# Performance work log

Hardware: AMD Instinct MI355X
Metric: run time of the kernel (lower is better)

Reference implementation:

```python
import jax, jax.numpy as jnp
import numpy as np
import math

N, D, H, O = 8192, 2048, 512, 32


def setup_inputs() -> dict:
    key = jax.random.key(0)
    k0, k1, k2, k3 = jax.random.split(key, 4)
    x = jax.random.normal(k0, (N, D), jnp.float32)
    y = jax.random.normal(k1, (N, O), jnp.float32)
    # kaiming_uniform fan_in / relu: bound = sqrt(6 / fan_in)
    b_w1 = math.sqrt(6.0 / D)
    W1 = jax.random.uniform(k2, (H, D), jnp.float32, -b_w1, b_w1)
    b1 = jnp.full((H,), 0.01, jnp.float32)
    # W = [final_layer.weight^T ; bias] -> (H+1, O)
    b_w2 = math.sqrt(6.0 / H)
    W = jax.random.uniform(k3, (H + 1, O), jnp.float32, -b_w2, b_w2)
    P = jnp.eye(H + 1, dtype=jnp.float32)  # P = 1 * I
    return {"x": x, "y": y, "W1": W1, "b1": b1, "W": W, "P": P, "epoch": 2}


def _rls(Phi, y, W, P):
    """Sequential Sherman-Morrison rank-1 updates (the torch per-sample loop) as lax.scan."""
    def step(carry, inp):
        W, P = carry
        xi, yi = inp                      # xi: (H+1,), yi: (O,)
        px = P @ xi                       # (H+1,)
        denom = 1.0 + xi @ px             # scalar 1 + xi P xi^T
        W = W - jnp.outer(px, xi @ W - yi) / denom
        P = P - jnp.outer(px, xi @ P) / denom
        return (W, P), None
    (W, P), _ = jax.lax.scan(step, (W, P), (Phi, y))
    return W, P


def reference(x, y, W1, b1, W, P, epoch):
    # feature_extractor: Linear + ReLU
    feature = jax.nn.relu(x @ W1.T + b1)                       # (N, H)
    ones_col = jnp.ones((feature.shape[0], 1), feature.dtype)
    Phi = jnp.concatenate([feature, ones_col], axis=1)         # (N, H+1)
    # RLS processes ceil(0.5**epoch * N) samples (deterministic prefix here)
    sample = math.ceil(0.5 ** epoch * Phi.shape[0])
    W_new, P_new = _rls(Phi[:sample], y[:sample], W, P)
    # final_layer with updated weights: out = feature @ W_new[:-1] + W_new[-1] == Phi @ W_new
    out = Phi @ W_new                                          # (N, O)
    return out
```

## Files before the change

kernel.cpp:

```cpp
#include <hip/hip_runtime.h>
#include <math.h>

#define NROWS 8192
#define DIN   2048
#define HF    512
#define NAUG  513
#define OOUT  32
#define SRLS  2048
#define LDP   576
#define NPAD  576

typedef short bf16x8 __attribute__((ext_vector_type(8)));
typedef float f32x4  __attribute__((ext_vector_type(4)));

__global__ __launch_bounds__(256) void split32(const float* __restrict__ s,
                                               unsigned short* __restrict__ hi,
                                               unsigned short* __restrict__ lo,
                                               int n4)
{
    int stride = gridDim.x * blockDim.x;
    for (int i = blockIdx.x * blockDim.x + threadIdx.x; i < n4; i += stride) {
        float4 v = ((const float4*)s)[i];
        float vv[4] = {v.x, v.y, v.z, v.w};
        ushort4 h, l;
        unsigned short hh[4], ll[4];
#pragma unroll
        for (int j = 0; j < 4; ++j) {
            unsigned int bits = __float_as_uint(vv[j]);
            float hf = __uint_as_float(bits & 0xFFFF0000u);
            float rf = vv[j] - hf;
            hh[j] = (unsigned short)(bits >> 16);
            ll[j] = (unsigned short)(__float_as_uint(rf) >> 16);
        }
        h.x = hh[0]; h.y = hh[1]; h.z = hh[2]; h.w = hh[3];
        l.x = ll[0]; l.y = ll[1]; l.z = ll[2]; l.w = ll[3];
        ((ushort4*)hi)[i] = h;
        ((ushort4*)lo)[i] = l;
    }
}

__device__ __forceinline__ void gl_lds16(const unsigned short* g, unsigned short* l)
{
    __builtin_amdgcn_global_load_lds(
        (const __attribute__((address_space(1))) unsigned int*)g,
        (__attribute__((address_space(3))) unsigned int*)l, 16, 0, 0);
}

__global__ __launch_bounds__(256) void phi_mfma(const unsigned short* __restrict__ Ahi,
                                                const unsigned short* __restrict__ Alo,
                                                const unsigned short* __restrict__ Bhi,
                                                const unsigned short* __restrict__ Blo,
                                                const float* __restrict__ b1,
                                                float* __restrict__ Phi)
{
    __shared__ unsigned short sAhi[128 * 32], sAlo[128 * 32];
    __shared__ unsigned short sBhi[64 * 32],  sBlo[64 * 32];
    const int tid = threadIdx.x;
    const int bx = blockIdx.x & 7;
    const int by = blockIdx.x >> 3;
    const int row0 = by * 128, col0 = bx * 64;
    const int wave = tid >> 6, lane = tid & 63;
    const int wr = wave >> 1, wc = wave & 1;
    const int sr = tid >> 2, sk = (tid & 3) * 8;

    f32x4 acc[4][2] = {};

    for (int k0 = 0; k0 < DIN; k0 += 32) {
        gl_lds16(&Ahi[(size_t)(row0 + sr) * DIN + k0 + sk],      &sAhi[sr * 32 + sk]);
        gl_lds16(&Ahi[(size_t)(row0 + 64 + sr) * DIN + k0 + sk], &sAhi[(64 + sr) * 32 + sk]);
        gl_lds16(&Alo[(size_t)(row0 + sr) * DIN + k0 + sk],      &sAlo[sr * 32 + sk]);
        gl_lds16(&Alo[(size_t)(row0 + 64 + sr) * DIN + k0 + sk], &sAlo[(64 + sr) * 32 + sk]);
        gl_lds16(&Bhi[(size_t)(col0 + sr) * DIN + k0 + sk],      &sBhi[sr * 32 + sk]);
        gl_lds16(&Blo[(size_t)(col0 + sr) * DIN + k0 + sk],      &sBlo[sr * 32 + sk]);
        __syncthreads();

        const int rA = lane & 15;
        const int ko = (lane >> 4) * 8;
        bf16x8 ah[4], al[4], bh[2], bl[2];
#pragma unroll
        for (int m = 0; m < 4; ++m) {
            int r = wr * 64 + m * 16 + rA;
            ah[m] = *(const bf16x8*)&sAhi[r * 32 + ko];
            al[m] = *(const bf16x8*)&sAlo[r * 32 + ko];
        }
#pragma unroll
        for (int n = 0; n < 2; ++n) {
            int cC = wc * 32 + n * 16 + rA;
            bh[n] = *(const bf16x8*)&sBhi[cC * 32 + ko];
            bl[n] = *(const bf16x8*)&sBlo[cC * 32 + ko];
        }
#pragma unroll
        for (int m = 0; m < 4; ++m)
#pragma unroll
            for (int n = 0; n < 2; ++n) {
                acc[m][n] = __builtin_amdgcn_mfma_f32_16x16x32_bf16(ah[m], bh[n], acc[m][n], 0, 0, 0);
                acc[m][n] = __builtin_amdgcn_mfma_f32_16x16x32_bf16(ah[m], bl[n], acc[m][n], 0, 0, 0);
                acc[m][n] = __builtin_amdgcn_mfma_f32_16x16x32_bf16(al[m], bh[n], acc[m][n], 0, 0, 0);
            }
        __syncthreads();
    }

#pragma unroll
    for (int n = 0; n < 2; ++n) {
        int col = col0 + wc * 32 + n * 16 + (lane & 15);
        float bb = b1[col];
#pragma unroll
        for (int m = 0; m < 4; ++m) {
            int rbase = row0 + wr * 64 + m * 16 + (lane >> 4) * 4;
#pragma unroll
            for (int r = 0; r < 4; ++r) {
                float v = acc[m][n][r] + bb;
                Phi[(size_t)(rbase + r) * LDP + col] = fmaxf(v, 0.0f);
            }
        }
    }
}

__global__ void aux_fill(const float* __restrict__ y, float* __restrict__ Phi)
{
    int idx = blockIdx.x * blockDim.x + threadIdx.x;
    int r = idx >> 6;
    int c = 512 + (idx & 63);
    float v = 0.0f;
    if (c == 512) v = 1.0f;
    else if (c >= 513 && c < 513 + OOUT && r < SRLS) v = y[r * OOUT + (c - 513)];
    Phi[(size_t)r * LDP + c] = v;
}

__global__ __launch_bounds__(256) void gram(const float* __restrict__ Phi,
                                            float* __restrict__ G)
{
    int bi = blockIdx.x / 18, bj = blockIdx.x % 18;
    if (bi > bj) return;
    __shared__ float Ta[32][33];
    __shared__ float Tb[32][33];
    const int tid = threadIdx.x;
    const int tx = tid & 15, ty = tid >> 4;
    const int i0 = bi * 32, j0 = bj * 32;
    double acc00 = 0., acc01 = 0., acc10 = 0., acc11 = 0.;

    for (int s0 = 0; s0 < SRLS; s0 += 32) {
        int r = tid >> 3, c4 = (tid & 7) * 4;
        float4 va = *(const float4*)&Phi[(size_t)(s0 + r) * LDP + i0 + c4];
        Ta[r][c4 + 0] = va.x; Ta[r][c4 + 1] = va.y;
        Ta[r][c4 + 2] = va.z; Ta[r][c4 + 3] = va.w;
        float4 vb = *(const float4*)&Phi[(size_t)(s0 + r) * LDP + j0 + c4];
        Tb[r][c4 + 0] = vb.x; Tb[r][c4 + 1] = vb.y;
        Tb[r][c4 + 2] = vb.z; Tb[r][c4 + 3] = vb.w;
        __syncthreads();
#pragma unroll
        for (int s = 0; s < 32; ++s) {
            double a0 = (double)Ta[s][ty * 2], a1 = (double)Ta[s][ty * 2 + 1];
            double b0 = (double)Tb[s][tx * 2], b1v = (double)Tb[s][tx * 2 + 1];
            acc00 += a0 * b0; acc01 += a0 * b1v;
            acc10 += a1 * b0; acc11 += a1 * b1v;
        }
        __syncthreads();
    }
    double accs[2][2] = {{acc00, acc01}, {acc10, acc11}};
#pragma unroll
    for (int ii = 0; ii < 2; ++ii)
#pragma unroll
        for (int jj = 0; jj < 2; ++jj) {
            int gi = i0 + ty * 2 + ii, gj = j0 + tx * 2 + jj;
            float v = (float)(accs[ii][jj] + ((gi == gj) ? 1.0 : 0.0));
            G[gi * NPAD + gj] = v;
            G[gj * NPAD + gi] = v;
        }
}

__global__ void gd_fill(const float* __restrict__ G, double* __restrict__ Gd)
{
    int idx = blockIdx.x * blockDim.x + threadIdx.x;
    int i = idx / NPAD, j = idx - i * NPAD;
    double v;
    if (i < NAUG && j < NAUG) v = (double)G[idx];
    else v = (i == j) ? 1.0 : 0.0;
    Gd[idx] = v;
}

__global__ void bd_fill(const float* __restrict__ G, const float* __restrict__ W0,
                        double* __restrict__ Bd)
{
    int idx = blockIdx.x * blockDim.x + threadIdx.x;
    int i = idx >> 5, c = idx & 31;
    double v = 0.0;
    if (i < NAUG) v = (double)G[i * NPAD + 513 + c] + (double)W0[i * OOUT + c];
    Bd[idx] = v;
}

__global__ __launch_bounds__(256) void chol_diag(double* __restrict__ Gd,
                                                 double* __restrict__ Dinv, int p)
{
    __shared__ double A[64][65];
    __shared__ double Zs[64][65];
    const int tid = threadIdx.x;
    const int r0g = p * 64;
    for (int idx = tid; idx < 4096; idx += 256) {
        int r = idx >> 6, c = idx & 63;
        A[r][c] = Gd[(size_t)(r0g + r) * NPAD + r0g + c];
    }
    __syncthreads();

    for (int kb = 0; kb < 8; ++kb) {
        const int k0 = kb * 8;
        if (tid < 64) {
            const int lane = tid;
            for (int k = k0; k < k0 + 8; ++k) {
                double d = A[k][k];
                double inv = 1.0 / sqrt(d);
                double lik = 0.0;
                if (lane == k)     A[k][k] = d * inv;
                else if (lane > k) { lik = A[lane][k] * inv; A[lane][k] = lik; }
                asm volatile("" ::: "memory");
                if (lane > k) {
                    for (int j = k + 1; j < k0 + 8; ++j)
                        A[lane][j] -= lik * A[j][k];
                }
                asm volatile("" ::: "memory");
            }
        }
        __syncthreads();
        if (k0 + 8 < 64) {
            const int i = tid >> 2, cg = tid & 3;
            if (i >= k0 + 8) {
                double lik[8];
#pragma unroll
                for (int k = 0; k < 8; ++k) lik[k] = A[i][k0 + k];
                for (int j = k0 + 8 + cg; j <= i; j += 4) {
                    double s = A[i][j];
#pragma unroll
                    for (int k = 0; k < 8; ++k) s -= lik[k] * A[j][k0 + k];
                    A[i][j] = s;
                }
            }
        }
        __syncthreads();
    }

    for (int rb = 0; rb < 8; ++rb) {
        const int r0 = rb * 8;
        const int c = tid & 63, pg = tid >> 6;
        double t0 = 0.0, t1 = 0.0;
        for (int q = 0; q < r0; ++q) {
            double zqc = Zs[q][c];
            t0 += A[r0 + pg][q] * zqc;
            t1 += A[r0 + pg + 4][q] * zqc;
        }
        Zs[r0 + pg][c]     = ((r0 + pg) == c ? 1.0 : 0.0) - t0;
        Zs[r0 + pg + 4][c] = ((r0 + pg + 4) == c ? 1.0 : 0.0) - t1;
        __syncthreads();
        if (tid < 64) {
            const int lane = tid;
            for (int q = 0; q < 8; ++q) {
                double v = Zs[r0 + q][lane];
                for (int w = 0; w < q; ++w) v -= A[r0 + q][r0 + w] * Zs[r0 + w][lane];
                Zs[r0 + q][lane] = v / A[r0 + q][r0 + q];
                asm volatile("" ::: "memory");
            }
        }
        __syncthreads();
    }

    for (int idx = tid; idx < 4096; idx += 256) {
        int r = idx >> 6, c = idx & 63;
        Gd[(size_t)(r0g + r) * NPAD + r0g + c] = A[r][c];
        Dinv[(size_t)p * 4096 + idx] = (c <= r) ? Zs[r][c] : 0.0;
    }
}

__global__ __launch_bounds__(256) void trsm(double* __restrict__ Gd,
                                            const double* __restrict__ Dinv, int p)
{
    __shared__ double As[64][65];
    __shared__ double Mi[64][65];
    const int tid = threadIdx.x;
    const int rb = p + 1 + blockIdx.x;
    const int d0 = p * 64, r0 = rb * 64;
    const double* Dv = Dinv + (size_t)p * 4096;
    for (int idx = tid; idx < 4096; idx += 256) {
        int r = idx >> 6, c = idx & 63;
        As[r][c] = Gd[(size_t)(r0 + r) * NPAD + d0 + c];
        Mi[r][c] = Dv[idx];
    }
    __syncthreads();
    const int tx = tid & 15, ty = tid >> 4;
    double acc[4][4] = {};
    for (int q = 0; q < 64; ++q) {
        double av[4], mv[4];
#pragma unroll
        for (int u = 0; u < 4; ++u) av[u] = As[ty * 4 + u][q];
#pragma unroll
        for (int v = 0; v < 4; ++v) mv[v] = Mi[tx * 4 + v][q];
#pragma unroll
        for (int u = 0; u < 4; ++u)
#pragma unroll
            for (int v = 0; v < 4; ++v) acc[u][v] += av[u] * mv[v];
    }
    __syncthreads();
#pragma unroll
    for (int u = 0; u < 4; ++u)
#pragma unroll
        for (int v = 0; v < 4; ++v)
            Gd[(size_t)(r0 + ty * 4 + u) * NPAD + d0 + tx * 4 + v] = acc[u][v];
}

__global__ __launch_bounds__(256) void syrk(double* __restrict__ Gd, int p)
{
    __shared__ double LiT[64][66];
    __shared__ double LjT[64][66];
    const int m = 8 - p;
    int b = blockIdx.x, jj = 0;
    while (b >= m - jj) { b -= m - jj; ++jj; }
    const int jb = p + 1 + jj, ib = jb + b;
    const int i0 = ib * 64, j0 = jb * 64, d0 = p * 64;
    const int tid = threadIdx.x;
    for (int idx = tid; idx < 4096; idx += 256) {
        int r = idx >> 6, c = idx & 63;
        LiT[c][r] = Gd[(size_t)(i0 + r) * NPAD + d0 + c];
        LjT[c][r] = Gd[(size_t)(j0 + r) * NPAD + d0 + c];
    }
    __syncthreads();
    const int tx = tid & 15, ty = tid >> 4;
    const int rr = ty * 4, cc = tx * 4;
    double acc[4][4] = {};
    for (int k = 0; k < 64; ++k) {
        double ai[4], aj[4];
#pragma unroll
        for (int q = 0; q < 4; ++q) ai[q] = LiT[k][rr + q];
#pragma unroll
        for (int q = 0; q < 4; ++q) aj[q] = LjT[k][cc + q];
#pragma unroll
        for (int q = 0; q < 4; ++q)
#pragma unroll
            for (int w = 0; w < 4; ++w) acc[q][w] += ai[q] * aj[w];
    }
#pragma unroll
    for (int q = 0; q < 4; ++q)
#pragma unroll
        for (int w = 0; w < 4; ++w) {
            size_t off = (size_t)(i0 + rr + q) * NPAD + j0 + cc + w;
            Gd[off] -= acc[q][w];
        }
}

__global__ __launch_bounds__(256) void mnprep(const double* __restrict__ Gd,
                                              const double* __restrict__ Dinv,
                                              double* __restrict__ Mb,
                                              double* __restrict__ Nb)
{
    __shared__ double Ls[64][65];
    __shared__ double Ds[64][65];
    int b = blockIdx.x;
    const bool doN = (b >= 36);
    if (doN) b -= 36;
    int jj = 0, rem = b;
    while (rem >= 8 - jj) { rem -= 8 - jj; ++jj; }
    const int ii = jj + 1 + rem;
    const int tid = threadIdx.x;
    const double* Dv = Dinv + (size_t)(doN ? ii : jj) * 4096;
    for (int idx = tid; idx < 4096; idx += 256) {
        int r = idx >> 6, c = idx & 63;
        Ls[r][c] = Gd[(size_t)(ii * 64 + r) * NPAD + jj * 64 + c];
        Ds[r][c] = Dv[idx];
    }
    __syncthreads();
    const int tx = tid & 15, ty = tid >> 4;
    double acc[4][4] = {};
    for (int k = 0; k < 64; ++k) {
        double a[4], bb[4];
        if (!doN) {
#pragma unroll
            for (int u = 0; u < 4; ++u) a[u]  = Ls[ty * 4 + u][k];
#pragma unroll
            for (int v = 0; v < 4; ++v) bb[v] = Ds[k][tx * 4 + v];
        } else {
#pragma unroll
            for (int u = 0; u < 4; ++u) a[u]  = Ds[ty * 4 + u][k];
#pragma unroll
            for (int v = 0; v < 4; ++v) bb[v] = Ls[k][tx * 4 + v];
        }
#pragma unroll
        for (int u = 0; u < 4; ++u)
#pragma unroll
            for (int v = 0; v < 4; ++v) acc[u][v] += a[u] * bb[v];
    }
    double* dst = (doN ? Nb : Mb) + (size_t)(ii * 9 + jj) * 4096;
#pragma unroll
    for (int u = 0; u < 4; ++u)
#pragma unroll
        for (int v = 0; v < 4; ++v)
            dst[(ty * 4 + u) * 64 + tx * 4 + v] = acc[u][v];
}

__global__ __launch_bounds__(256) void fwd_step(const double* __restrict__ Mb,
                                                double* __restrict__ Bd, int j)
{
    __shared__ double Ms[64][65];
    __shared__ double Bj[64][33];
    const int i = j + 1 + blockIdx.x;
    const int tid = threadIdx.x;
    const double* Mblk = Mb + (size_t)(i * 9 + j) * 4096;
    for (int idx = tid; idx < 4096; idx += 256) Ms[idx >> 6][idx & 63] = Mblk[idx];
    for (int idx = tid; idx < 2048; idx += 256) Bj[idx >> 5][idx & 31] = Bd[j * 2048 + idx];
    __syncthreads();
    const int c = tid & 31, rg = tid >> 5;
    double acc[8] = {};
    for (int k = 0; k < 64; ++k) {
        double bk = Bj[k][c];
#pragma unroll
        for (int u = 0; u < 8; ++u) acc[u] += Ms[rg * 8 + u][k] * bk;
    }
#pragma unroll
    for (int u = 0; u < 8; ++u)
        Bd[(size_t)(i * 64 + rg * 8 + u) * 32 + c] -= acc[u];
}

__global__ __launch_bounds__(256) void ydiag(const double* __restrict__ Dinv,
                                             double* __restrict__ Bd)
{
    __shared__ double Ds[64][65];
    __shared__ double Bi[64][33];
    const int i = blockIdx.x;
    const int tid = threadIdx.x;
    const double* Dv = Dinv + (size_t)i * 4096;
    for (int idx = tid; idx < 4096; idx += 256) Ds[idx >> 6][idx & 63] = Dv[idx];
    for (int idx = tid; idx < 2048; idx += 256) Bi[idx >> 5][idx & 31] = Bd[i * 2048 + idx];
    __syncthreads();
    const int c = tid & 31, rg = tid >> 5;
    double acc[8] = {};
    for (int k = 0; k < 64; ++k) {
        double bk = Bi[k][c];
#pragma unroll
        for (int u = 0; u < 8; ++u) acc[u] += Ds[rg * 8 + u][k] * bk;
    }
#pragma unroll
    for (int u = 0; u < 8; ++u)
        Bd[(size_t)(i * 64 + rg * 8 + u) * 32 + c] = acc[u];
}

__global__ __launch_bounds__(256) void bwd_step(const double* __restrict__ Nb,
                                                double* __restrict__ Bd, int q)
{
    __shared__ double Ns[64][65];
    __shared__ double Bq[64][33];
    const int i = blockIdx.x;
    const int tid = threadIdx.x;
    const double* Nblk = Nb + (size_t)(q * 9 + i) * 4096;
    for (int idx = tid; idx < 4096; idx += 256) Ns[idx >> 6][idx & 63] = Nblk[idx];
    for (int idx = tid; idx < 2048; idx += 256) Bq[idx >> 5][idx & 31] = Bd[q * 2048 + idx];
    __syncthreads();
    const int c = tid & 31, rg = tid >> 5;
    double acc[8] = {};
    for (int k = 0; k < 64; ++k) {
        double bk = Bq[k][c];
#pragma unroll
        for (int u = 0; u < 8; ++u) acc[u] += Ns[k][rg * 8 + u] * bk;
    }
#pragma unroll
    for (int u = 0; u < 8; ++u)
        Bd[(size_t)(i * 64 + rg * 8 + u) * 32 + c] -= acc[u];
}

__global__ __launch_bounds__(256) void xfinal(const double* __restrict__ Dinv,
                                              const double* __restrict__ Bd,
                                              float* __restrict__ Xs)
{
    __shared__ double Ds[64][65];
    __shared__ double Bi[64][33];
    const int i = blockIdx.x;
    const int tid = threadIdx.x;
    const double* Dv = Dinv + (size_t)i * 4096;
    for (int idx = tid; idx < 4096; idx += 256) Ds[idx >> 6][idx & 63] = Dv[idx];
    for (int idx = tid; idx < 2048; idx += 256) Bi[idx >> 5][idx & 31] = Bd[i * 2048 + idx];
    __syncthreads();
    const int c = tid & 31, rg = tid >> 5;
    double acc[8] = {};
    for (int k = 0; k < 64; ++k) {
        double bk = Bi[k][c];
#pragma unroll
        for (int u = 0; u < 8; ++u) acc[u] += Ds[k][rg * 8 + u] * bk;
    }
#pragma unroll
    for (int u = 0; u < 8; ++u) {
        int gi = i * 64 + rg * 8 + u;
        if (gi < NAUG) Xs[gi * 32 + c] = (float)acc[u];
    }
}

__global__ __launch_bounds__(256) void out_gemm(const float* __restrict__ Phi,
                                                const float* __restrict__ Xs,
                                                float* __restrict__ outp)
{
    __shared__ float sX[NAUG * 32];
    const int tid = threadIdx.x;
    for (int i2 = tid; i2 < NAUG * 32; i2 += 256) sX[i2] = Xs[i2];
    __syncthreads();
    int rt = tid >> 5, c = tid & 31;
    int i0 = blockIdx.x * 32;
    for (int i = i0 + rt; i < i0 + 32; i += 8) {
        const float* prow = &Phi[(size_t)i * LDP];
        float acc = 0.0f;
        for (int k = 0; k < 512; k += 4) {
            float4 p = *(const float4*)&prow[k];
            acc = fmaf(p.x, sX[(k + 0) * 32 + c], acc);
            acc = fmaf(p.y, sX[(k + 1) * 32 + c], acc);
            acc = fmaf(p.z, sX[(k + 2) * 32 + c], acc);
            acc = fmaf(p.w, sX[(k + 3) * 32 + c], acc);
        }
        acc = fmaf(prow[512], sX[512 * 32 + c], acc);
        outp[(size_t)i * 32 + c] = acc;
    }
}

extern "C" void kernel_launch(void* const* d_in, const int* in_sizes, int n_in,
                              void* d_out, int out_size, void* d_ws, size_t ws_size,
                              hipStream_t stream)
{
    const float* x  = (const float*)d_in[0];
    const float* y  = (const float*)d_in[1];
    const float* W1 = (const float*)d_in[2];
    const float* b1 = (const float*)d_in[3];
    const float* W0 = (const float*)d_in[4];

    char* base = (char*)d_ws;
    float*  Phi  = (float*)base;
    float*  G    = (float*)(base + 18874368);
    double* Gd   = (double*)(base + 20201472);
    double* Bd   = (double*)(base + 22855680);
    double* Dinv = (double*)(base + 23003136);
    float*  Xs   = (float*)(base + 23298048);
    double* Mb   = (double*)(base + 23367680);
    double* Nb   = (double*)(base + 26021888);
    unsigned short* xhi = (unsigned short*)(base + 28676096);
    unsigned short* xlo = (unsigned short*)(base + 62230528);
    unsigned short* whi = (unsigned short*)(base + 95784960);
    unsigned short* wlo = (unsigned short*)(base + 97882112);
    float* outp = (float*)d_out;

    split32<<<2048, 256, 0, stream>>>(x,  xhi, xlo, NROWS * DIN / 4);
    split32<<<1024, 256, 0, stream>>>(W1, whi, wlo, HF * DIN / 4);
    phi_mfma<<<512, 256, 0, stream>>>(xhi, xlo, whi, wlo, b1, Phi);
    aux_fill<<<(NROWS * 64) / 256, 256, 0, stream>>>(y, Phi);
    gram<<<18 * 18, 256, 0, stream>>>(Phi, G);
    gd_fill<<<(NPAD * NPAD) / 256, 256, 0, stream>>>(G, Gd);
    bd_fill<<<(NPAD * 32) / 256, 256, 0, stream>>>(G, W0, Bd);
    for (int p = 0; p < 9; ++p) {
        chol_diag<<<1, 256, 0, stream>>>(Gd, Dinv, p);
        int m = 8 - p;
        if (m > 0) {
            trsm<<<m, 256, 0, stream>>>(Gd, Dinv, p);
            syrk<<<m * (m + 1) / 2, 256, 0, stream>>>(Gd, p);
        }
    }
    mnprep<<<72, 256, 0, stream>>>(Gd, Dinv, Mb, Nb);
    for (int j = 0; j < 8; ++j)
        fwd_step<<<8 - j, 256, 0, stream>>>(Mb, Bd, j);
    ydiag<<<9, 256, 0, stream>>>(Dinv, Bd);
    for (int q = 8; q >= 1; --q)
        bwd_step<<<q, 256, 0, stream>>>(Nb, Bd, q);
    xfinal<<<9, 256, 0, stream>>>(Dinv, Bd, Xs);
    out_gemm<<<NROWS / 32, 256, 0, stream>>>(Phi, Xs, outp);
}
```

Baseline: 1.121 ms.

## Split gram across sample chunks, fuse trsm+syrk, single-kernel triangular sweeps

The Gram matrix is now computed as 8 sample-chunk partials over lower-triangle tiles plus a y-projection tile, then reduced in a separate kernel straight into the double-precision buffer. This replaces the serial single-pass gram and its conversion kernels. The per-panel trsm and syrk launches are fused into one panel_up kernel that keeps the L blocks in a separate buffer. The diagonal Cholesky factor uses shuffles and register arrays. The forward and backward block sweeps, previously about 18 small launches, become one 1024-thread kernel, trading launch overhead for single-CU serial execution.

```diff
diff --git a/kernel.cpp b/kernel.cpp
--- a/kernel.cpp
+++ b/kernel.cpp
@@ -116,35 +116,47 @@
     }
 }
 
-__global__ void aux_fill(const float* __restrict__ y, float* __restrict__ Phi)
+__global__ void aux_fill(float* __restrict__ Phi)
+{
+    int r = blockIdx.x * blockDim.x + threadIdx.x;
+    if (r < NROWS) Phi[(size_t)r * LDP + 512] = 1.0f;
+}
+
+__global__ void gd_init(double* __restrict__ Gd)
 {
     int idx = blockIdx.x * blockDim.x + threadIdx.x;
-    int r = idx >> 6;
-    int c = 512 + (idx & 63);
-    float v = 0.0f;
-    if (c == 512) v = 1.0f;
-    else if (c >= 513 && c < 513 + OOUT && r < SRLS) v = y[r * OOUT + (c - 513)];
-    Phi[(size_t)r * LDP + c] = v;
-}
-
-__global__ __launch_bounds__(256) void gram(const float* __restrict__ Phi,
-                                            float* __restrict__ G)
-{
-    int bi = blockIdx.x / 18, bj = blockIdx.x % 18;
-    if (bi > bj) return;
+    int i = idx / NPAD, j = idx - i * NPAD;
+    Gd[idx] = (i == j) ? 1.0 : 0.0;
+}
+
+__global__ __launch_bounds__(256) void gram_part(const float* __restrict__ Phi,
+                                                 const float* __restrict__ y,
+                                                 double* __restrict__ Gp)
+{
+    const int pr = blockIdx.x % 170;
+    const int ch = blockIdx.x / 170;
     __shared__ float Ta[32][33];
     __shared__ float Tb[32][33];
     const int tid = threadIdx.x;
     const int tx = tid & 15, ty = tid >> 4;
-    const int i0 = bi * 32, j0 = bj * 32;
+    int i0, j0; bool ytile;
+    if (pr < 153) {
+        int rem = pr, bj = 0;
+        while (rem >= 17 - bj) { rem -= 17 - bj; ++bj; }
+        int bi = bj + rem;
+        i0 = bi * 32; j0 = bj * 32; ytile = false;
+    } else {
+        i0 = (pr - 153) * 32; j0 = 0; ytile = true;
+    }
     double acc00 = 0., acc01 = 0., acc10 = 0., acc11 = 0.;
-
-    for (int s0 = 0; s0 < SRLS; s0 += 32) {
+    const int sBase = ch * 256;
+    for (int s0 = sBase; s0 < sBase + 256; s0 += 32) {
         int r = tid >> 3, c4 = (tid & 7) * 4;
         float4 va = *(const float4*)&Phi[(size_t)(s0 + r) * LDP + i0 + c4];
         Ta[r][c4 + 0] = va.x; Ta[r][c4 + 1] = va.y;
         Ta[r][c4 + 2] = va.z; Ta[r][c4 + 3] = va.w;
-        float4 vb = *(const float4*)&Phi[(size_t)(s0 + r) * LDP + j0 + c4];
+        float4 vb = ytile ? *(const float4*)&y[(size_t)(s0 + r) * 32 + c4]
+                          : *(const float4*)&Phi[(size_t)(s0 + r) * LDP + j0 + c4];
         Tb[r][c4 + 0] = vb.x; Tb[r][c4 + 1] = vb.y;
         Tb[r][c4 + 2] = vb.z; Tb[r][c4 + 3] = vb.w;
         __syncthreads();
@@ -157,36 +169,42 @@
         }
         __syncthreads();
     }
+    size_t base = ((size_t)pr * 8 + ch) * 1024;
     double accs[2][2] = {{acc00, acc01}, {acc10, acc11}};
 #pragma unroll
     for (int ii = 0; ii < 2; ++ii)
 #pragma unroll
-        for (int jj = 0; jj < 2; ++jj) {
-            int gi = i0 + ty * 2 + ii, gj = j0 + tx * 2 + jj;
-            float v = (float)(accs[ii][jj] + ((gi == gj) ? 1.0 : 0.0));
-            G[gi * NPAD + gj] = v;
-            G[gj * NPAD + gi] = v;
-        }
-}
-
-__global__ void gd_fill(const float* __restrict__ G, double* __restrict__ Gd)
-{
-    int idx = blockIdx.x * blockDim.x + threadIdx.x;
-    int i = idx / NPAD, j = idx - i * NPAD;
-    double v;
-    if (i < NAUG && j < NAUG) v = (double)G[idx];
-    else v = (i == j) ? 1.0 : 0.0;
-    Gd[idx] = v;
-}
-
-__global__ void bd_fill(const float* __restrict__ G, const float* __restrict__ W0,
-                        double* __restrict__ Bd)
-{
-    int idx = blockIdx.x * blockDim.x + threadIdx.x;
-    int i = idx >> 5, c = idx & 31;
-    double v = 0.0;
-    if (i < NAUG) v = (double)G[i * NPAD + 513 + c] + (double)W0[i * OOUT + c];
-    Bd[idx] = v;
+        for (int jj = 0; jj < 2; ++jj)
+            Gp[base + (size_t)(ty * 2 + ii) * 32 + tx * 2 + jj] = accs[ii][jj];
+}
+
+__global__ __launch_bounds__(256) void gram_reduce(const double* __restrict__ Gp,
+                                                   double* __restrict__ Gd,
+                                                   double* __restrict__ By)
+{
+    const int pr = blockIdx.x;
+    const int tid = threadIdx.x;
+    for (int e = tid; e < 1024; e += 256) {
+        double s = 0.0;
+#pragma unroll
+        for (int ch = 0; ch < 8; ++ch)
+            s += Gp[((size_t)pr * 8 + ch) * 1024 + e];
+        int er = e >> 5, ec = e & 31;
+        if (pr < 153) {
+            int rem = pr, bj = 0;
+            while (rem >= 17 - bj) { rem -= 17 - bj; ++bj; }
+            int bi = bj + rem;
+            int gi = bi * 32 + er, gj = bj * 32 + ec;
+            if (gi < NAUG && gj < NAUG) {
+                double v = s + ((gi == gj) ? 1.0 : 0.0);
+                Gd[(size_t)gi * NPAD + gj] = v;
+                if (bi != bj) Gd[(size_t)gj * NPAD + gi] = v;
+            }
+        } else {
+            int gi = (pr - 153) * 32 + er;
+            if (gi < NAUG) By[gi * 32 + ec] = s;
+        }
+    }
 }
 
 __global__ __launch_bounds__(256) void chol_diag(double* __restrict__ Gd,
@@ -194,6 +212,7 @@
 {
     __shared__ double A[64][65];
     __shared__ double Zs[64][65];
+    __shared__ double L8[8][9];
     const int tid = threadIdx.x;
     const int r0g = p * 64;
     for (int idx = tid; idx < 4096; idx += 256) {
@@ -204,35 +223,56 @@
 
     for (int kb = 0; kb < 8; ++kb) {
         const int k0 = kb * 8;
-        if (tid < 64) {
-            const int lane = tid;
-            for (int k = k0; k < k0 + 8; ++k) {
-                double d = A[k][k];
-                double inv = 1.0 / sqrt(d);
-                double lik = 0.0;
-                if (lane == k)     A[k][k] = d * inv;
-                else if (lane > k) { lik = A[lane][k] * inv; A[lane][k] = lik; }
-                asm volatile("" ::: "memory");
-                if (lane > k) {
-                    for (int j = k + 1; j < k0 + 8; ++j)
-                        A[lane][j] -= lik * A[j][k];
+        if (tid < 8) {
+            const int r = tid;
+            double a[8];
+#pragma unroll
+            for (int c = 0; c < 8; ++c) a[c] = A[k0 + r][k0 + c];
+#pragma unroll
+            for (int k = 0; k < 8; ++k) {
+                double dk = __shfl(a[k], k, 64);
+                double s  = sqrt(dk);
+                double inv = 1.0 / s;
+                if (r == k) a[k] = s;
+                else if (r > k) a[k] *= inv;
+                double lrk = a[k];
+#pragma unroll
+                for (int j = k + 1; j < 8; ++j) {
+                    double ljk = __shfl(a[k], j, 64);
+                    if (r >= j) a[j] -= lrk * ljk;
                 }
-                asm volatile("" ::: "memory");
-            }
-        }
-        __syncthreads();
-        if (k0 + 8 < 64) {
-            const int i = tid >> 2, cg = tid & 3;
-            if (i >= k0 + 8) {
-                double lik[8];
-#pragma unroll
-                for (int k = 0; k < 8; ++k) lik[k] = A[i][k0 + k];
-                for (int j = k0 + 8 + cg; j <= i; j += 4) {
-                    double s = A[i][j];
-#pragma unroll
-                    for (int k = 0; k < 8; ++k) s -= lik[k] * A[j][k0 + k];
-                    A[i][j] = s;
-                }
+            }
+#pragma unroll
+            for (int c = 0; c < 8; ++c) {
+                L8[r][c] = (c <= r) ? a[c] : 0.0;
+                A[k0 + r][k0 + c] = a[c];
+            }
+        }
+        __syncthreads();
+        const int iRow = k0 + 8 + (tid >> 2);
+        const int cg = tid & 3;
+        double l[8];
+        if (iRow < 64) {
+#pragma unroll
+            for (int k = 0; k < 8; ++k) l[k] = A[iRow][k0 + k];
+#pragma unroll
+            for (int k = 0; k < 8; ++k) {
+                l[k] /= L8[k][k];
+#pragma unroll
+                for (int j = k + 1; j < 8; ++j) l[j] -= l[k] * L8[j][k];
+            }
+            if (cg == 0) {
+#pragma unroll
+                for (int k = 0; k < 8; ++k) A[iRow][k0 + k] = l[k];
+            }
+        }
+        __syncthreads();
+        if (iRow < 64) {
+            for (int j = k0 + 8 + cg; j <= iRow; j += 4) {
+                double s = A[iRow][j];
+#pragma unroll
+                for (int k = 0; k < 8; ++k) s -= l[k] * A[j][k0 + k];
+                A[iRow][j] = s;
             }
         }
         __syncthreads();
@@ -251,13 +291,17 @@
         Zs[r0 + pg + 4][c] = ((r0 + pg + 4) == c ? 1.0 : 0.0) - t1;
         __syncthreads();
         if (tid < 64) {
-            const int lane = tid;
+            double z[8];
+#pragma unroll
+            for (int q = 0; q < 8; ++q) z[q] = Zs[r0 + q][tid];
+#pragma unroll
             for (int q = 0; q < 8; ++q) {
-                double v = Zs[r0 + q][lane];
-                for (int w = 0; w < q; ++w) v -= A[r0 + q][r0 + w] * Zs[r0 + w][lane];
-                Zs[r0 + q][lane] = v / A[r0 + q][r0 + q];
-                asm volatile("" ::: "memory");
-            }
+#pragma unroll
+                for (int w = 0; w < q; ++w) z[q] -= A[r0 + q][r0 + w] * z[w];
+                z[q] /= A[r0 + q][r0 + q];
+            }
+#pragma unroll
+            for (int q = 0; q < 8; ++q) Zs[r0 + q][tid] = z[q];
         }
         __syncthreads();
     }
@@ -269,82 +313,85 @@
     }
 }
 
-__global__ __launch_bounds__(256) void trsm(double* __restrict__ Gd,
-                                            const double* __restrict__ Dinv, int p)
-{
-    __shared__ double As[64][65];
-    __shared__ double Mi[64][65];
-    const int tid = threadIdx.x;
-    const int rb = p + 1 + blockIdx.x;
-    const int d0 = p * 64, r0 = rb * 64;
-    const double* Dv = Dinv + (size_t)p * 4096;
-    for (int idx = tid; idx < 4096; idx += 256) {
-        int r = idx >> 6, c = idx & 63;
-        As[r][c] = Gd[(size_t)(r0 + r) * NPAD + d0 + c];
-        Mi[r][c] = Dv[idx];
-    }
-    __syncthreads();
-    const int tx = tid & 15, ty = tid >> 4;
-    double acc[4][4] = {};
-    for (int q = 0; q < 64; ++q) {
-        double av[4], mv[4];
-#pragma unroll
-        for (int u = 0; u < 4; ++u) av[u] = As[ty * 4 + u][q];
-#pragma unroll
-        for (int v = 0; v < 4; ++v) mv[v] = Mi[tx * 4 + v][q];
-#pragma unroll
-        for (int u = 0; u < 4; ++u)
-#pragma unroll
-            for (int v = 0; v < 4; ++v) acc[u][v] += av[u] * mv[v];
-    }
-    __syncthreads();
-#pragma unroll
-    for (int u = 0; u < 4; ++u)
-#pragma unroll
-        for (int v = 0; v < 4; ++v)
-            Gd[(size_t)(r0 + ty * 4 + u) * NPAD + d0 + tx * 4 + v] = acc[u][v];
-}
-
-__global__ __launch_bounds__(256) void syrk(double* __restrict__ Gd, int p)
-{
-    __shared__ double LiT[64][66];
-    __shared__ double LjT[64][66];
+__global__ __launch_bounds__(256) void panel_up(double* __restrict__ Gd,
+                                                const double* __restrict__ Dinv,
+                                                double* __restrict__ Lmat, int p)
+{
+    __shared__ double Dv[64][65];
+    __shared__ double Ai[64][65];
+    __shared__ double Aj[64][65];
     const int m = 8 - p;
     int b = blockIdx.x, jj = 0;
     while (b >= m - jj) { b -= m - jj; ++jj; }
-    const int jb = p + 1 + jj, ib = jb + b;
-    const int i0 = ib * 64, j0 = jb * 64, d0 = p * 64;
-    const int tid = threadIdx.x;
+    const int jB = p + 1 + jj, iB = jB + b;
+    const int d0 = p * 64, i0 = iB * 64, j0 = jB * 64;
+    const int tid = threadIdx.x;
+    const bool diag = (iB == jB);
+    const double* Dp = Dinv + (size_t)p * 4096;
     for (int idx = tid; idx < 4096; idx += 256) {
-        int r = idx >> 6, c = idx & 63;
-        LiT[c][r] = Gd[(size_t)(i0 + r) * NPAD + d0 + c];
-        LjT[c][r] = Gd[(size_t)(j0 + r) * NPAD + d0 + c];
+        int r = idx >> 6, cc = idx & 63;
+        Dv[r][cc] = Dp[idx];
+        Ai[r][cc] = Gd[(size_t)(i0 + r) * NPAD + d0 + cc];
+        if (!diag) Aj[r][cc] = Gd[(size_t)(j0 + r) * NPAD + d0 + cc];
     }
     __syncthreads();
     const int tx = tid & 15, ty = tid >> 4;
-    const int rr = ty * 4, cc = tx * 4;
+    double li[4][4] = {}, lj[4][4] = {};
+    for (int q = 0; q < 64; ++q) {
+        double dvq[4], av[4];
+#pragma unroll
+        for (int v = 0; v < 4; ++v) dvq[v] = Dv[tx * 4 + v][q];
+#pragma unroll
+        for (int u = 0; u < 4; ++u) av[u] = Ai[ty * 4 + u][q];
+#pragma unroll
+        for (int u = 0; u < 4; ++u)
+#pragma unroll
+            for (int v = 0; v < 4; ++v) li[u][v] += av[u] * dvq[v];
+        if (!diag) {
+#pragma unroll
+            for (int u = 0; u < 4; ++u) av[u] = Aj[ty * 4 + u][q];
+#pragma unroll
+            for (int u = 0; u < 4; ++u)
+#pragma unroll
+                for (int v = 0; v < 4; ++v) lj[u][v] += av[u] * dvq[v];
+        }
+    }
+    __syncthreads();
+#pragma unroll
+    for (int u = 0; u < 4; ++u)
+#pragma unroll
+        for (int v = 0; v < 4; ++v) {
+            Ai[ty * 4 + u][tx * 4 + v] = li[u][v];
+            if (!diag) Aj[ty * 4 + u][tx * 4 + v] = lj[u][v];
+        }
+    __syncthreads();
+    if (jj == 0) {
+        double* dst = Lmat + ((size_t)iB * 9 + p) * 4096;
+        for (int idx = tid; idx < 4096; idx += 256)
+            dst[idx] = Ai[idx >> 6][idx & 63];
+    }
     double acc[4][4] = {};
-    for (int k = 0; k < 64; ++k) {
-        double ai[4], aj[4];
-#pragma unroll
-        for (int q = 0; q < 4; ++q) ai[q] = LiT[k][rr + q];
-#pragma unroll
-        for (int q = 0; q < 4; ++q) aj[q] = LjT[k][cc + q];
-#pragma unroll
-        for (int q = 0; q < 4; ++q)
-#pragma unroll
-            for (int w = 0; w < 4; ++w) acc[q][w] += ai[q] * aj[w];
-    }
-#pragma unroll
-    for (int q = 0; q < 4; ++q)
-#pragma unroll
-        for (int w = 0; w < 4; ++w) {
-            size_t off = (size_t)(i0 + rr + q) * NPAD + j0 + cc + w;
-            Gd[off] -= acc[q][w];
-        }
-}
-
-__global__ __launch_bounds__(256) void mnprep(const double* __restrict__ Gd,
+    for (int q = 0; q < 64; ++q) {
+        double a_[4], b_[4];
+#pragma unroll
+        for (int u = 0; u < 4; ++u) a_[u] = Ai[ty * 4 + u][q];
+#pragma unroll
+        for (int v = 0; v < 4; ++v) b_[v] = diag ? Ai[tx * 4 + v][q] : Aj[tx * 4 + v][q];
+#pragma unroll
+        for (int u = 0; u < 4; ++u)
+#pragma unroll
+            for (int v = 0; v < 4; ++v) acc[u][v] += a_[u] * b_[v];
+    }
+#pragma unroll
+    for (int u = 0; u < 4; ++u)
+#pragma unroll
+        for (int v = 0; v < 4; ++v) {
+            size_t off = (size_t)(i0 + ty * 4 + u) * NPAD + j0 + tx * 4 + v;
+            Gd[off] -= acc[u][v];
+        }
+}
+
+__global__ __launch_bounds__(256) void mnprep(const double* __restrict__ Lmat,
                                               const double* __restrict__ Dinv,
                                               double* __restrict__ Mb,
                                               double* __restrict__ Nb)
@@ -359,10 +406,10 @@
     const int ii = jj + 1 + rem;
     const int tid = threadIdx.x;
     const double* Dv = Dinv + (size_t)(doN ? ii : jj) * 4096;
+    const double* Lsrc = Lmat + ((size_t)ii * 9 + jj) * 4096;
     for (int idx = tid; idx < 4096; idx += 256) {
-        int r = idx >> 6, c = idx & 63;
-        Ls[r][c] = Gd[(size_t)(ii * 64 + r) * NPAD + jj * 64 + c];
-        Ds[r][c] = Dv[idx];
+        Ls[idx >> 6][idx & 63] = Lsrc[idx];
+        Ds[idx >> 6][idx & 63] = Dv[idx];
     }
     __syncthreads();
     const int tx = tid & 15, ty = tid >> 4;
@@ -393,98 +440,89 @@
             dst[(ty * 4 + u) * 64 + tx * 4 + v] = acc[u][v];
 }
 
-__global__ __launch_bounds__(256) void fwd_step(const double* __restrict__ Mb,
-                                                double* __restrict__ Bd, int j)
-{
-    __shared__ double Ms[64][65];
-    __shared__ double Bj[64][33];
-    const int i = j + 1 + blockIdx.x;
-    const int tid = threadIdx.x;
-    const double* Mblk = Mb + (size_t)(i * 9 + j) * 4096;
-    for (int idx = tid; idx < 4096; idx += 256) Ms[idx >> 6][idx & 63] = Mblk[idx];
-    for (int idx = tid; idx < 2048; idx += 256) Bj[idx >> 5][idx & 31] = Bd[j * 2048 + idx];
-    __syncthreads();
+__global__ __launch_bounds__(1024) void sweep_all(const double* __restrict__ Mb,
+                                                  const double* __restrict__ Nb,
+                                                  const double* __restrict__ Dinv,
+                                                  const double* __restrict__ By,
+                                                  const float* __restrict__ W0,
+                                                  float* __restrict__ Xs)
+{
+    __shared__ double Bl[NPAD][32];
+    const int tid = threadIdx.x;
     const int c = tid & 31, rg = tid >> 5;
-    double acc[8] = {};
-    for (int k = 0; k < 64; ++k) {
-        double bk = Bj[k][c];
-#pragma unroll
-        for (int u = 0; u < 8; ++u) acc[u] += Ms[rg * 8 + u][k] * bk;
-    }
-#pragma unroll
-    for (int u = 0; u < 8; ++u)
-        Bd[(size_t)(i * 64 + rg * 8 + u) * 32 + c] -= acc[u];
-}
-
-__global__ __launch_bounds__(256) void ydiag(const double* __restrict__ Dinv,
-                                             double* __restrict__ Bd)
-{
-    __shared__ double Ds[64][65];
-    __shared__ double Bi[64][33];
-    const int i = blockIdx.x;
-    const int tid = threadIdx.x;
-    const double* Dv = Dinv + (size_t)i * 4096;
-    for (int idx = tid; idx < 4096; idx += 256) Ds[idx >> 6][idx & 63] = Dv[idx];
-    for (int idx = tid; idx < 2048; idx += 256) Bi[idx >> 5][idx & 31] = Bd[i * 2048 + idx];
-    __syncthreads();
-    const int c = tid & 31, rg = tid >> 5;
-    double acc[8] = {};
-    for (int k = 0; k < 64; ++k) {
-        double bk = Bi[k][c];
-#pragma unroll
-        for (int u = 0; u < 8; ++u) acc[u] += Ds[rg * 8 + u][k] * bk;
-    }
-#pragma unroll
-    for (int u = 0; u < 8; ++u)
-        Bd[(size_t)(i * 64 + rg * 8 + u) * 32 + c] = acc[u];
-}
-
-__global__ __launch_bounds__(256) void bwd_step(const double* __restrict__ Nb,
-                                                double* __restrict__ Bd, int q)
-{
-    __shared__ double Ns[64][65];
-    __shared__ double Bq[64][33];
-    const int i = blockIdx.x;
-    const int tid = threadIdx.x;
-    const double* Nblk = Nb + (size_t)(q * 9 + i) * 4096;
-    for (int idx = tid; idx < 4096; idx += 256) Ns[idx >> 6][idx & 63] = Nblk[idx];
-    for (int idx = tid; idx < 2048; idx += 256) Bq[idx >> 5][idx & 31] = Bd[q * 2048 + idx];
-    __syncthreads();
-    const int c = tid & 31, rg = tid >> 5;
-    double acc[8] = {};
-    for (int k = 0; k < 64; ++k) {
-        double bk = Bq[k][c];
-#pragma unroll
-        for (int u = 0; u < 8; ++u) acc[u] += Ns[k][rg * 8 + u] * bk;
-    }
-#pragma unroll
-    for (int u = 0; u < 8; ++u)
-        Bd[(size_t)(i * 64 + rg * 8 + u) * 32 + c] -= acc[u];
-}
-
-__global__ __launch_bounds__(256) void xfinal(const double* __restrict__ Dinv,
-                                              const double* __restrict__ Bd,
-                                              float* __restrict__ Xs)
-{
-    __shared__ double Ds[64][65];
-    __shared__ double Bi[64][33];
-    const int i = blockIdx.x;
-    const int tid = threadIdx.x;
-    const double* Dv = Dinv + (size_t)i * 4096;
-    for (int idx = tid; idx < 4096; idx += 256) Ds[idx >> 6][idx & 63] = Dv[idx];
-    for (int idx = tid; idx < 2048; idx += 256) Bi[idx >> 5][idx & 31] = Bd[i * 2048 + idx];
-    __syncthreads();
-    const int c = tid & 31, rg = tid >> 5;
-    double acc[8] = {};
-    for (int k = 0; k < 64; ++k) {
-        double bk = Bi[k][c];
-#pragma unroll
-        for (int u = 0; u < 8; ++u) acc[u] += Ds[k][rg * 8 + u] * bk;
-    }
-#pragma unroll
-    for (int u = 0; u < 8; ++u) {
-        int gi = i * 64 + rg * 8 + u;
-        if (gi < NAUG) Xs[gi * 32 + c] = (float)acc[u];
+
+    for (int i = rg; i < NPAD; i += 32)
+        Bl[i][c] = (i < NAUG) ? (double)W0[i * 32 + c] + By[i * 32 + c] : 0.0;
+    __syncthreads();
+
+    for (int j = 0; j < 8; ++j) {
+        for (int bi2 = j + 1; bi2 <= 8; ++bi2) {
+            const double* Mblk = Mb + ((size_t)bi2 * 9 + j) * 4096;
+            double a0 = 0.0, a1 = 0.0;
+            for (int k = 0; k < 64; ++k) {
+                double bk = Bl[j * 64 + k][c];
+                a0 += Mblk[rg * 64 + k] * bk;
+                a1 += Mblk[(rg + 32) * 64 + k] * bk;
+            }
+            Bl[bi2 * 64 + rg][c]      -= a0;
+            Bl[bi2 * 64 + rg + 32][c] -= a1;
+        }
+        __syncthreads();
+    }
+    {
+        double r0v[9], r1v[9];
+#pragma unroll
+        for (int i2 = 0; i2 < 9; ++i2) {
+            const double* Dv = Dinv + (size_t)i2 * 4096;
+            double a0 = 0.0, a1 = 0.0;
+            for (int k = 0; k < 64; ++k) {
+                double bk = Bl[i2 * 64 + k][c];
+                a0 += Dv[rg * 64 + k] * bk;
+                a1 += Dv[(rg + 32) * 64 + k] * bk;
+            }
+            r0v[i2] = a0; r1v[i2] = a1;
+        }
+        __syncthreads();
+#pragma unroll
+        for (int i2 = 0; i2 < 9; ++i2) {
+            Bl[i2 * 64 + rg][c]      = r0v[i2];
+            Bl[i2 * 64 + rg + 32][c] = r1v[i2];
+        }
+        __syncthreads();
+    }
+    for (int q = 8; q >= 1; --q) {
+        for (int i2 = 0; i2 < q; ++i2) {
+            const double* Nblk = Nb + ((size_t)q * 9 + i2) * 4096;
+            double a0 = 0.0, a1 = 0.0;
+            for (int k = 0; k < 64; ++k) {
+                double bk = Bl[q * 64 + k][c];
+                a0 += Nblk[k * 64 + rg] * bk;
+                a1 += Nblk[k * 64 + rg + 32] * bk;
+            }
+            Bl[i2 * 64 + rg][c]      -= a0;
+            Bl[i2 * 64 + rg + 32][c] -= a1;
+        }
+        __syncthreads();
+    }
+    {
+        double r0v[9], r1v[9];
+#pragma unroll
+        for (int i2 = 0; i2 < 9; ++i2) {
+            const double* Dv = Dinv + (size_t)i2 * 4096;
+            double a0 = 0.0, a1 = 0.0;
+            for (int k = 0; k < 64; ++k) {
+                double bk = Bl[i2 * 64 + k][c];
+                a0 += Dv[k * 64 + rg] * bk;
+                a1 += Dv[k * 64 + rg + 32] * bk;
+            }
+            r0v[i2] = a0; r1v[i2] = a1;
+        }
+#pragma unroll
+        for (int i2 = 0; i2 < 9; ++i2) {
+            int gi0 = i2 * 64 + rg, gi1 = i2 * 64 + rg + 32;
+            if (gi0 < NAUG) Xs[gi0 * 32 + c] = (float)r0v[i2];
+            if (gi1 < NAUG) Xs[gi1 * 32 + c] = (float)r1v[i2];
+        }
     }
 }
 
@@ -525,9 +563,8 @@
 
     char* base = (char*)d_ws;
     float*  Phi  = (float*)base;
-    float*  G    = (float*)(base + 18874368);
     double* Gd   = (double*)(base + 20201472);
-    double* Bd   = (double*)(base + 22855680);
+    double* By   = (double*)(base + 22855680);
     double* Dinv = (double*)(base + 23003136);
     float*  Xs   = (float*)(base + 23298048);
     double* Mb   = (double*)(base + 23367680);
@@ -536,29 +573,24 @@
     unsigned short* xlo = (unsigned short*)(base + 62230528);
     unsigned short* whi = (unsigned short*)(base + 95784960);
     unsigned short* wlo = (unsigned short*)(base + 97882112);
+    double* Gp   = (double*)(base + 28676096);
+    double* Lmat = (double*)(base + 39817216);
     float* outp = (float*)d_out;
 
     split32<<<2048, 256, 0, stream>>>(x,  xhi, xlo, NROWS * DIN / 4);
     split32<<<1024, 256, 0, stream>>>(W1, whi, wlo, HF * DIN / 4);
     phi_mfma<<<512, 256, 0, stream>>>(xhi, xlo, whi, wlo, b1, Phi);
-    aux_fill<<<(NROWS * 64) / 256, 256, 0, stream>>>(y, Phi);
-    gram<<<18 * 18, 256, 0, stream>>>(Phi, G);
-    gd_fill<<<(NPAD * NPAD) / 256, 256, 0, stream>>>(G, Gd);
-    bd_fill<<<(NPAD * 32) / 256, 256, 0, stream>>>(G, W0, Bd);
+    aux_fill<<<32, 256, 0, stream>>>(Phi);
+    gd_init<<<(NPAD * NPAD) / 256, 256, 0, stream>>>(Gd);
+    gram_part<<<170 * 8, 256, 0, stream>>>(Phi, y, Gp);
+    gram_reduce<<<170, 256, 0, stream>>>(Gp, Gd, By);
     for (int p = 0; p < 9; ++p) {
         chol_diag<<<1, 256, 0, stream>>>(Gd, Dinv, p);
         int m = 8 - p;
-        if (m > 0) {
-            trsm<<<m, 256, 0, stream>>>(Gd, Dinv, p);
-            syrk<<<m * (m + 1) / 2, 256, 0, stream>>>(Gd, p);
-        }
-    }
-    mnprep<<<72, 256, 0, stream>>>(Gd, Dinv, Mb, Nb);
-    for (int j = 0; j < 8; ++j)
-        fwd_step<<<8 - j, 256, 0, stream>>>(Mb, Bd, j);
-    ydiag<<<9, 256, 0, stream>>>(Dinv, Bd);
-    for (int q = 8; q >= 1; --q)
-        bwd_step<<<q, 256, 0, stream>>>(Nb, Bd, q);
-    xfinal<<<9, 256, 0, stream>>>(Dinv, Bd, Xs);
+        if (m > 0)
+            panel_up<<<m * (m + 1) / 2, 256, 0, stream>>>(Gd, Dinv, Lmat, p);
+    }
+    mnprep<<<72, 256, 0, stream>>>(Lmat, Dinv, Mb, Nb);
+    sweep_all<<<1, 1024, 0, stream>>>(Mb, Nb, Dinv, By, W0, Xs);
     out_gemm<<<NROWS / 32, 256, 0, stream>>>(Phi, Xs, outp);
 }
```

Result: slower. 2.497 ms (+122.8%).
